# Performance work log

Hardware: AMD Instinct MI355X
Metric: run time of the kernel (lower is better)

## Reference

```python
import jax, jax.numpy as jnp
import numpy as np

B, S, D, H = 2, 2048, 2048, 16
HD = D // H


def setup_inputs() -> dict:
    key = jax.random.key(0)
    ks = jax.random.split(key, 11)
    scale = 1.0 / np.sqrt(D)
    causal = jnp.tril(jnp.ones((S, S), dtype=bool))
    attention_mask = jnp.broadcast_to(causal, (B, H, S, S))
    return {
        "queries": jax.random.normal(ks[0], (B, S, D), dtype=jnp.float32),
        "keys": jax.random.normal(ks[1], (B, S, D), dtype=jnp.float32),
        "values": jax.random.normal(ks[2], (B, S, D), dtype=jnp.float32),
        "attention_mask": attention_mask,
        "wq": jax.random.normal(ks[3], (D, D), dtype=jnp.float32) * scale,
        "bq": jax.random.normal(ks[4], (D,), dtype=jnp.float32) * 0.01,
        "wk": jax.random.normal(ks[5], (D, D), dtype=jnp.float32) * scale,
        "bk": jax.random.normal(ks[6], (D,), dtype=jnp.float32) * 0.01,
        "wv": jax.random.normal(ks[7], (D, D), dtype=jnp.float32) * scale,
        "bv": jax.random.normal(ks[8], (D,), dtype=jnp.float32) * 0.01,
        "wo": jax.random.normal(ks[9], (D, D), dtype=jnp.float32) * scale,
        "bo": jax.random.normal(ks[10], (D,), dtype=jnp.float32) * 0.01,
    }


def _split_heads(x):
    # (B, S, D) -> (B, H, S, HD)
    b, s, _ = x.shape
    return x.reshape(b, s, H, HD).transpose(0, 2, 1, 3)


def reference(queries, keys, values, attention_mask, wq, bq, wk, bk, wv, bv, wo, bo):
    # Linear layers (torch convention: x @ W.T + b)
    q = _split_heads(queries @ wq.T + bq)   # (B, H, S, HD)
    k = _split_heads(keys @ wk.T + bk)
    v = _split_heads(values @ wv.T + bv)

    inv_sqrt_d = 1.0 / jnp.sqrt(jnp.asarray(HD, dtype=q.dtype))
    scores = jnp.einsum('bhqd,bhkd->bhqk', q, k) * inv_sqrt_d  # (B, H, S, S)
    scores = jnp.where(attention_mask, scores, jnp.asarray(-jnp.inf, dtype=scores.dtype))
    probs = jax.nn.softmax(scores, axis=-1)
    out = jnp.einsum('bhqk,bhkd->bhqd', probs, v)              # (B, H, S, HD)

    out = out.transpose(0, 2, 1, 3).reshape(queries.shape[0], queries.shape[1], D)
    return out @ wo.T + bo
```

## Files before the change

### kernel.cpp

```cpp
#include <hip/hip_runtime.h>
#include <hip/hip_bf16.h>

typedef unsigned short u16;
typedef __bf16 bf16x8 __attribute__((ext_vector_type(8)));
typedef short  short8 __attribute__((ext_vector_type(8)));
typedef float  f32x4  __attribute__((ext_vector_type(4)));
typedef float  f32x16 __attribute__((ext_vector_type(16)));
typedef u16    u16x4  __attribute__((ext_vector_type(4)));

#define BB 2
#define SS 2048
#define DD 2048
#define HH 16
#define HDIM 128
#define MM (BB * SS)
#define KSCALE 0.12752039505554602f

static __device__ __forceinline__ f32x4 mfma16(short8 a, short8 b, f32x4 c) {
    return __builtin_amdgcn_mfma_f32_16x16x32_bf16(
        __builtin_bit_cast(bf16x8, a), __builtin_bit_cast(bf16x8, b), c, 0, 0, 0);
}

static __device__ __forceinline__ f32x16 mfma32(short8 a, short8 b, f32x16 c) {
    return __builtin_amdgcn_mfma_f32_32x32x16_bf16(
        __builtin_bit_cast(bf16x8, a), __builtin_bit_cast(bf16x8, b), c, 0, 0, 0);
}

static __device__ __forceinline__ u16 f2bf(float f) {
    union { float f; unsigned u; } v; v.f = f;
    unsigned r = v.u + 0x7fffu + ((v.u >> 16) & 1u);
    return (u16)(r >> 16);
}

static __device__ __forceinline__ float bf2f(u16 v) {
    union { unsigned u; float f; } t; t.u = ((unsigned)v) << 16;
    return t.f;
}

static __device__ __forceinline__ uint4 pack8(float4 a, float4 b) {
    uint4 o;
    o.x = (unsigned)f2bf(a.x) | ((unsigned)f2bf(a.y) << 16);
    o.y = (unsigned)f2bf(a.z) | ((unsigned)f2bf(a.w) << 16);
    o.z = (unsigned)f2bf(b.x) | ((unsigned)f2bf(b.y) << 16);
    o.w = (unsigned)f2bf(b.z) | ((unsigned)f2bf(b.w) << 16);
    return o;
}

static __device__ __forceinline__ void gload_lds16(const u16* g, u16* l) {
    __builtin_amdgcn_global_load_lds(
        (const __attribute__((address_space(1))) unsigned int*)g,
        (__attribute__((address_space(3))) unsigned int*)l, 16, 0, 0);
}

__global__ __launch_bounds__(256) void conv_all(
    const float* __restrict__ q, const float* __restrict__ k, const float* __restrict__ v,
    const float* __restrict__ wq, const float* __restrict__ wk,
    const float* __restrict__ wv, const float* __restrict__ wo,
    u16* __restrict__ out)
{
    constexpr int n1 = MM * DD / 8;
    constexpr int nw = DD * DD / 8;
    constexpr int total = 3 * n1 + 4 * nw;
    const int stride = gridDim.x * blockDim.x;
    for (int i = blockIdx.x * blockDim.x + threadIdx.x; i < total; i += stride) {
        const float* s; int j = i; float sc = 1.f;
        if (j < n1)            { s = q; }
        else if (j < 2 * n1)   { s = k;  j -= n1; }
        else if (j < 3 * n1)   { s = v;  j -= 2 * n1; }
        else {
            j -= 3 * n1;
            if (j < nw)        { s = wq; sc = KSCALE; }
            else if (j < 2*nw) { s = wk; j -= nw; }
            else if (j < 3*nw) { s = wv; j -= 2 * nw; }
            else               { s = wo; j -= 3 * nw; }
        }
        const float4* sp = (const float4*)s + (size_t)j * 2;
        float4 a = sp[0], bb2 = sp[1];
        a.x *= sc; a.y *= sc; a.z *= sc; a.w *= sc;
        bb2.x *= sc; bb2.y *= sc; bb2.z *= sc; bb2.w *= sc;
        ((uint4*)out)[i] = pack8(a, bb2);
    }
}

__global__ __launch_bounds__(256, 3) void gemm_qkv(
    const u16* __restrict__ A0, const u16* __restrict__ W0,
    const float* __restrict__ bq, const float* __restrict__ bk,
    const float* __restrict__ bv, u16* __restrict__ C0)
{
    __shared__ u16 S[128 * 132];
    u16* Al = S;
    u16* Bl = S + 4096;

    const int z = blockIdx.z;
    const u16* A  = A0 + (size_t)z * MM * DD;
    const u16* Wb = W0 + (size_t)z * DD * DD;
    const float* bias = (z == 0) ? bq : (z == 1 ? bk : bv);
    const float bsc = (z == 0) ? KSCALE : 1.f;

    const int tid = threadIdx.x;
    const int lane = tid & 63;
    const int lg = lane >> 4, li = lane & 15;
    const int wid = tid >> 6;
    const int brow = blockIdx.x * 128, bcol = blockIdx.y * 128;
    const int wm = wid >> 1, wn = wid & 1;

    const int srow = tid >> 2;
    const int scol = (tid & 3) * 8;

    const f32x4 zero = {0.f, 0.f, 0.f, 0.f};
    f32x4 acc[4][4];
#pragma unroll
    for (int i = 0; i < 4; ++i)
#pragma unroll
        for (int j = 0; j < 4; ++j) acc[i][j] = zero;

    const u16* aptr = A  + (size_t)(brow + srow) * DD + scol;
    const u16* bptr = Wb + (size_t)(bcol + srow) * DD + scol;
    const size_t half = (size_t)64 * DD;

    for (int kt = 0; kt < DD; kt += 32) {
        gload_lds16(aptr + kt,        &Al[tid * 8]);
        gload_lds16(aptr + half + kt, &Al[2048 + tid * 8]);
        gload_lds16(bptr + kt,        &Bl[tid * 8]);
        gload_lds16(bptr + half + kt, &Bl[2048 + tid * 8]);
        __syncthreads();

        short8 af[4], bf[4];
#pragma unroll
        for (int mi = 0; mi < 4; ++mi)
            af[mi] = *(const short8*)(&Al[(wm * 64 + mi * 16 + li) * 32 + lg * 8]);
#pragma unroll
        for (int ni = 0; ni < 4; ++ni)
            bf[ni] = *(const short8*)(&Bl[(wn * 64 + ni * 16 + li) * 32 + lg * 8]);
#pragma unroll
        for (int mi = 0; mi < 4; ++mi)
#pragma unroll
            for (int ni = 0; ni < 4; ++ni)
                acc[mi][ni] = mfma16(af[mi], bf[ni], acc[mi][ni]);
        __syncthreads();
    }

    if (z == 2) {
        u16* Cl = S;
#pragma unroll
        for (int ni = 0; ni < 4; ++ni) {
            const int cc = wn * 64 + ni * 16 + li;
            const float bvv = bias[bcol + cc];
#pragma unroll
            for (int mi = 0; mi < 4; ++mi)
#pragma unroll
                for (int r = 0; r < 4; ++r) {
                    const int rr = wm * 64 + mi * 16 + lg * 4 + r;
                    Cl[cc * 132 + rr] = f2bf(acc[mi][ni][r] + bvv);
                }
        }
        __syncthreads();
        const int row = tid >> 1;
        const int hcol = (tid & 1) * 64;
        u16* dst = C0 + (size_t)2 * MM * DD + (size_t)(bcol + row) * MM + brow + hcol;
#pragma unroll
        for (int c = 0; c < 8; ++c)
            *(short8*)(dst + c * 8) = *(const short8*)(&Cl[row * 132 + hcol + c * 8]);
    } else {
        u16* Cp = C0 + (size_t)z * MM * DD;
#pragma unroll
        for (int ni = 0; ni < 4; ++ni) {
            const int col = bcol + wn * 64 + ni * 16 + li;
            const float bvv = bias[col] * bsc;
#pragma unroll
            for (int mi = 0; mi < 4; ++mi)
#pragma unroll
                for (int r = 0; r < 4; ++r) {
                    const int row = brow + wm * 64 + mi * 16 + lg * 4 + r;
                    Cp[(size_t)row * DD + col] = f2bf(acc[mi][ni][r] + bvv);
                }
        }
    }
}

__global__ __launch_bounds__(256) void gemm_out(
    const u16* __restrict__ A, const u16* __restrict__ Wb,
    const float* __restrict__ bias, float* __restrict__ Cp)
{
    __shared__ u16 Al[128 * 32];
    __shared__ u16 Bl[128 * 32];

    const int tid = threadIdx.x;
    const int lane = tid & 63;
    const int lg = lane >> 4, li = lane & 15;
    const int wid = tid >> 6;
    const int brow = blockIdx.x * 128, bcol = blockIdx.y * 128;
    const int wm = wid >> 1, wn = wid & 1;

    const int srow = tid >> 2;
    const int scol = (tid & 3) * 8;

    const f32x4 zero = {0.f, 0.f, 0.f, 0.f};
    f32x4 acc[4][4];
#pragma unroll
    for (int i = 0; i < 4; ++i)
#pragma unroll
        for (int j = 0; j < 4; ++j) acc[i][j] = zero;

    const u16* aptr = A  + (size_t)(brow + srow) * DD + scol;
    const u16* bptr = Wb + (size_t)(bcol + srow) * DD + scol;
    const size_t half = (size_t)64 * DD;

    for (int kt = 0; kt < DD; kt += 32) {
        gload_lds16(aptr + kt,        &Al[tid * 8]);
        gload_lds16(aptr + half + kt, &Al[2048 + tid * 8]);
        gload_lds16(bptr + kt,        &Bl[tid * 8]);
        gload_lds16(bptr + half + kt, &Bl[2048 + tid * 8]);
        __syncthreads();

        short8 af[4], bf[4];
#pragma unroll
        for (int mi = 0; mi < 4; ++mi)
            af[mi] = *(const short8*)(&Al[(wm * 64 + mi * 16 + li) * 32 + lg * 8]);
#pragma unroll
        for (int ni = 0; ni < 4; ++ni)
            bf[ni] = *(const short8*)(&Bl[(wn * 64 + ni * 16 + li) * 32 + lg * 8]);
#pragma unroll
        for (int mi = 0; mi < 4; ++mi)
#pragma unroll
            for (int ni = 0; ni < 4; ++ni)
                acc[mi][ni] = mfma16(af[mi], bf[ni], acc[mi][ni]);
        __syncthreads();
    }

#pragma unroll
    for (int ni = 0; ni < 4; ++ni) {
        const int col = bcol + wn * 64 + ni * 16 + li;
        const float bvv = bias[col];
#pragma unroll
        for (int mi = 0; mi < 4; ++mi)
#pragma unroll
            for (int r = 0; r < 4; ++r) {
                const int row = brow + wm * 64 + mi * 16 + lg * 4 + r;
                Cp[(size_t)row * DD + col] = acc[mi][ni][r] + bvv;
            }
    }
}

__global__ __launch_bounds__(256) void flash_attn(
    const u16* __restrict__ Q, const u16* __restrict__ Kp,
    const u16* __restrict__ Vt, u16* __restrict__ O,
    u16* __restrict__ PartO, float* __restrict__ PartML)
{
    constexpr int SP = 72;
    __shared__ u16 lds[16384 + 4 * 32 * SP];
    u16* Kl = lds;
    u16* Vl = lds + 8192;
    u16* Pl = lds + 16384;

    const int tid = threadIdx.x;
    const int wid = tid >> 6, lane = tid & 63;
    const int l5 = lane & 31;
    const int hi = lane >> 5;
    const int h = blockIdx.y, b = blockIdx.z;

    const int f = 39 - (int)blockIdx.x;
    int qt, ch;
    if (f < 4)       { qt = f;               ch = 0; }
    else if (f < 12) { int g = f - 4;  qt = 4  + (g >> 1); ch = g & 1; }
    else if (f < 24) { int g = f - 12; qt = 8  + g / 3;    ch = g % 3; }
    else             { int g = f - 24; qt = 12 + (g >> 2); ch = g & 3; }
    const int j0 = ch * 8;
    const int j1 = min(j0 + 8, 2 * qt + 2);
    const int qbase = qt * 128 + wid * 32;
    const int qg = qbase + l5;

    const int rK0 = tid >> 4, wK0 = tid & 15;
    const int bK0 = ((wK0 * 16) ^ ((rK0 & 7) << 4)) >> 1;
    const int rV0 = tid >> 3, wV0 = tid & 7;
    const int bV0 = ((wV0 * 16) ^ ((rV0 & 7) << 4)) >> 1;
    const u16* kbase = Kp + (size_t)(b * SS + rK0) * DD + h * HDIM + bK0;
    const u16* vbase = Vt + (size_t)(h * HDIM + rV0) * MM + b * SS + bV0;

    short8 qf[8];
    {
        const u16* qp0 = Q + (size_t)(b * SS + qg) * DD + h * HDIM + hi * 8;
#pragma unroll
        for (int ks = 0; ks < 8; ++ks)
            qf[ks] = *(const short8*)(qp0 + ks * 16);
    }

    float m_r = -__builtin_inff(), l_r = 0.f;
    f32x16 accO[4];
#pragma unroll
    for (int d = 0; d < 4; ++d) accO[d] = (f32x16)(0.f);

    for (int j = j0; j < j1; ++j) {
#pragma unroll
        for (int i_ = 0; i_ < 4; ++i_) {
            gload_lds16(kbase + (size_t)(j * 64 + i_ * 16) * DD, &Kl[(i_ * 256 + tid) * 8]);
            gload_lds16(vbase + (size_t)(i_ * 32) * MM + j * 64, &Vl[(i_ * 256 + tid) * 8]);
        }
        __syncthreads();

        if (j * 64 <= qbase + 31) {
            f32x16 accS[2];
            accS[0] = (f32x16)(0.f); accS[1] = (f32x16)(0.f);
            __builtin_amdgcn_s_setprio(1);
#pragma unroll
            for (int ks = 0; ks < 8; ++ks) {
#pragma unroll
                for (int kvb = 0; kvb < 2; ++kvb) {
                    const int row = kvb * 32 + l5;
                    const int e = (ks * 16 + hi * 8) ^ ((row & 7) << 3);
                    short8 kf = *(const short8*)(&Kl[row * 128 + e]);
                    accS[kvb] = mfma32(kf, qf[ks], accS[kvb]);
                }
            }
            __builtin_amdgcn_s_setprio(0);

            const bool domask = (j * 64 + 63 > qbase);
            float rmax = -__builtin_inff();
#pragma unroll
            for (int kvb = 0; kvb < 2; ++kvb)
#pragma unroll
                for (int r = 0; r < 16; ++r) {
                    float t = accS[kvb][r];
                    const int kv = j * 64 + kvb * 32 + (r & 3) + 8 * (r >> 2) + 4 * hi;
                    if (domask && kv > qg) t = -__builtin_inff();
                    accS[kvb][r] = t;
                    rmax = fmaxf(rmax, t);
                }
            rmax = fmaxf(rmax, __shfl_xor(rmax, 32, 64));

            if (!__all(rmax - m_r <= 11.5f)) {
                const float mn = fmaxf(m_r, rmax);
                const float sf = exp2f(m_r - mn);
                m_r = mn;
                l_r *= sf;
#pragma unroll
                for (int db = 0; db < 4; ++db) accO[db] = accO[db] * sf;
            }

            float ls = 0.f;
#pragma unroll
            for (int kvb = 0; kvb < 2; ++kvb)
#pragma unroll
                for (int r = 0; r < 16; ++r) {
                    const float e = exp2f(accS[kvb][r] - m_r);
                    accS[kvb][r] = e;
                    ls += e;
                }
            ls += __shfl_xor(ls, 32, 64);
            l_r += ls;

#pragma unroll
            for (int kvb = 0; kvb < 2; ++kvb)
#pragma unroll
                for (int g = 0; g < 4; ++g) {
                    u16x4 pk;
                    pk.x = f2bf(accS[kvb][g * 4 + 0]);
                    pk.y = f2bf(accS[kvb][g * 4 + 1]);
                    pk.z = f2bf(accS[kvb][g * 4 + 2]);
                    pk.w = f2bf(accS[kvb][g * 4 + 3]);
                    *(u16x4*)(&Pl[(wid * 32 + l5) * SP + kvb * 32 + g * 8 + hi * 4]) = pk;
                }

            __builtin_amdgcn_s_setprio(1);
#pragma unroll
            for (int ks = 0; ks < 4; ++ks) {
                short8 pf = *(const short8*)(&Pl[(wid * 32 + l5) * SP + ks * 16 + hi * 8]);
#pragma unroll
                for (int db = 0; db < 4; ++db) {
                    const int row = db * 32 + l5;
                    const int e = (ks * 16 + hi * 8) ^ ((row & 7) << 3);
                    short8 vf = *(const short8*)(&Vl[row * 64 + e]);
                    accO[db] = mfma32(vf, pf, accO[db]);
                }
            }
            __builtin_amdgcn_s_setprio(0);
        }
        __syncthreads();
    }

    if (f >= 4) {
        const int pslot = (b * HH + h) * 36 + (f - 4);
        u16* po = PartO + (size_t)pslot * 16384 + (size_t)(wid * 32 + l5) * 128;
#pragma unroll
        for (int db = 0; db < 4; ++db)
#pragma unroll
            for (int g = 0; g < 4; ++g) {
                const int d0 = db * 32 + g * 8 + hi * 4;
                u16x4 pk;
                pk.x = f2bf(accO[db][g * 4 + 0]);
                pk.y = f2bf(accO[db][g * 4 + 1]);
                pk.z = f2bf(accO[db][g * 4 + 2]);
                pk.w = f2bf(accO[db][g * 4 + 3]);
                *(u16x4*)(po + d0) = pk;
            }
        if (lane < 32) {
            float* ml = PartML + (size_t)pslot * 256;
            ml[wid * 32 + l5]       = m_r;
            ml[128 + wid * 32 + l5] = l_r;
        }
    } else {
        const float linv = 1.f / l_r;
        u16* Wl = lds + wid * 4096;
#pragma unroll
        for (int db = 0; db < 4; ++db)
#pragma unroll
            for (int g = 0; g < 4; ++g) {
                const int d0 = db * 32 + g * 8 + hi * 4;
                u16x4 pk;
                pk.x = f2bf(accO[db][g * 4 + 0] * linv);
                pk.y = f2bf(accO[db][g * 4 + 1] * linv);
                pk.z = f2bf(accO[db][g * 4 + 2] * linv);
                pk.w = f2bf(accO[db][g * 4 + 3] * linv);
                *(u16x4*)(&Wl[l5 * 128 + (d0 ^ ((l5 & 7) << 4))]) = pk;
            }
        const int q_l = lane >> 1;
        const int d0r = (lane & 1) * 64;
        u16* op = O + (size_t)(b * SS + qt * 128 + wid * 32 + q_l) * DD + h * HDIM + d0r;
#pragma unroll
        for (int c = 0; c < 8; ++c) {
            short8 vv = *(const short8*)(&Wl[q_l * 128 + ((d0r + c * 8) ^ ((q_l & 7) << 4))]);
            *(short8*)(op + c * 8) = vv;
        }
    }
}

__global__ __launch_bounds__(256) void attn_combine(
    const u16* __restrict__ PartO, const float* __restrict__ PartML,
    u16* __restrict__ O)
{
    const int qt = 4 + (int)blockIdx.x;
    const int h = blockIdx.y, b = blockIdx.z;
    const int nch = qt / 4 + 1;
    int f0m4;
    if (qt < 8)       f0m4 = (qt - 4) * 2;
    else if (qt < 12) f0m4 = 8 + (qt - 8) * 3;
    else              f0m4 = 20 + (qt - 12) * 4;
    const int pbase = (b * HH + h) * 36 + f0m4;

    const int tid = threadIdx.x;
    const int q = tid & 127;
    const int d0 = (tid >> 7) * 64;

    float mc[4], lc[4];
#pragma unroll
    for (int c = 0; c < 4; ++c) {
        if (c < nch) {
            mc[c] = PartML[(size_t)(pbase + c) * 256 + q];
            lc[c] = PartML[(size_t)(pbase + c) * 256 + 128 + q];
        } else { mc[c] = -__builtin_inff(); lc[c] = 0.f; }
    }
    float M = fmaxf(fmaxf(mc[0], mc[1]), fmaxf(mc[2], mc[3]));
    float wc[4], L = 0.f;
#pragma unroll
    for (int c = 0; c < 4; ++c) { wc[c] = exp2f(mc[c] - M); L += wc[c] * lc[c]; }
    const float Linv = 1.f / L;

    float acc[64];
#pragma unroll
    for (int i = 0; i < 64; ++i) acc[i] = 0.f;
#pragma unroll
    for (int c = 0; c < 4; ++c) {
        if (c < nch) {
            const float w = wc[c] * Linv;
            const u16* po = PartO + (size_t)(pbase + c) * 16384 + (size_t)q * 128 + d0;
#pragma unroll
            for (int i = 0; i < 64; ++i)
                acc[i] += w * bf2f(po[i]);
        }
    }

    u16* op = O + (size_t)(b * SS + qt * 128 + q) * DD + h * HDIM + d0;
#pragma unroll
    for (int j = 0; j < 8; ++j) {
        short8 vv;
#pragma unroll
        for (int e = 0; e < 8; ++e) vv[e] = (short)f2bf(acc[j * 8 + e]);
        *(short8*)(op + j * 8) = vv;
    }
}

extern "C" void kernel_launch(void* const* d_in, const int* in_sizes, int n_in,
                              void* d_out, int out_size, void* d_ws, size_t ws_size,
                              hipStream_t stream)
{
    const float* queries = (const float*)d_in[0];
    const float* keys    = (const float*)d_in[1];
    const float* values  = (const float*)d_in[2];
    const float* wq = (const float*)d_in[4];
    const float* bq = (const float*)d_in[5];
    const float* wk = (const float*)d_in[6];
    const float* bk = (const float*)d_in[7];
    const float* wv = (const float*)d_in[8];
    const float* bv = (const float*)d_in[9];
    const float* wo = (const float*)d_in[10];
    const float* bo = (const float*)d_in[11];

    const int NMD = MM * DD;
    const int NWW = DD * DD;

    u16* qb  = (u16*)d_ws;
    u16* wqb = qb  + (size_t)3 * NMD;
    u16* wob = wqb + (size_t)3 * NWW;
    u16* qw  = wob + (size_t)NWW;
    u16* aw  = qw  + (size_t)3 * NMD;
    u16*   partO  = qb;
    float* partML = (float*)wqb;
    (void)in_sizes; (void)n_in; (void)out_size; (void)ws_size;

    dim3 blk(256);
    dim3 gridC(2048);
    dim3 gridQKV(MM / 128, DD / 128, 3);
    dim3 gridO(MM / 128, DD / 128);
    dim3 gridA(40, HH, BB);
    dim3 gridX(12, HH, BB);

    conv_all<<<gridC, blk, 0, stream>>>(queries, keys, values, wq, wk, wv, wo, qb);
    gemm_qkv<<<gridQKV, blk, 0, stream>>>(qb, wqb, bq, bk, bv, qw);
    flash_attn<<<gridA, blk, 0, stream>>>(qw, qw + (size_t)NMD, qw + (size_t)2 * NMD, aw,
                                          partO, partML);
    attn_combine<<<gridX, blk, 0, stream>>>(partO, partML, aw);
    gemm_out<<<gridO, blk, 0, stream>>>(aw, wob, bo, (float*)d_out);
}
```

Measured before the change: 350.8 us.

## Keep P in registers via permlane32 swap and use hardware bf16 pack conversion

```diff
diff --git a/kernel.cpp b/kernel.cpp
--- a/kernel.cpp
+++ b/kernel.cpp
@@ -7,6 +7,7 @@
 typedef float  f32x4  __attribute__((ext_vector_type(4)));
 typedef float  f32x16 __attribute__((ext_vector_type(16)));
 typedef u16    u16x4  __attribute__((ext_vector_type(4)));
+typedef unsigned uintx2 __attribute__((ext_vector_type(2)));
 
 #define BB 2
 #define SS 2048
@@ -35,6 +36,16 @@
 static __device__ __forceinline__ float bf2f(u16 v) {
     union { unsigned u; float f; } t; t.u = ((unsigned)v) << 16;
     return t.f;
+}
+
+static __device__ __forceinline__ unsigned cvtpk(float lo, float hi) {
+    unsigned r;
+    asm("v_cvt_pk_bf16_f32 %0, %1, %2" : "=v"(r) : "v"(lo), "v"(hi));
+    return r;
+}
+
+static __device__ __forceinline__ void plswap(unsigned &a, unsigned &b) {
+    asm("v_permlane32_swap_b32 %0, %1" : "+v"(a), "+v"(b));
 }
 
 static __device__ __forceinline__ uint4 pack8(float4 a, float4 b) {
@@ -247,11 +258,9 @@
     const u16* __restrict__ Vt, u16* __restrict__ O,
     u16* __restrict__ PartO, float* __restrict__ PartML)
 {
-    constexpr int SP = 72;
-    __shared__ u16 lds[16384 + 4 * 32 * SP];
+    __shared__ u16 lds[16384];
     u16* Kl = lds;
     u16* Vl = lds + 8192;
-    u16* Pl = lds + 16384;
 
     const int tid = threadIdx.x;
     const int wid = tid >> 6, lane = tid & 63;
@@ -316,16 +325,24 @@
 
             const bool domask = (j * 64 + 63 > qbase);
             float rmax = -__builtin_inff();
-#pragma unroll
-            for (int kvb = 0; kvb < 2; ++kvb)
-#pragma unroll
-                for (int r = 0; r < 16; ++r) {
-                    float t = accS[kvb][r];
-                    const int kv = j * 64 + kvb * 32 + (r & 3) + 8 * (r >> 2) + 4 * hi;
-                    if (domask && kv > qg) t = -__builtin_inff();
-                    accS[kvb][r] = t;
-                    rmax = fmaxf(rmax, t);
-                }
+            if (domask) {
+#pragma unroll
+                for (int kvb = 0; kvb < 2; ++kvb)
+#pragma unroll
+                    for (int r = 0; r < 16; ++r) {
+                        float t = accS[kvb][r];
+                        const int kv = j * 64 + kvb * 32 + (r & 3) + 8 * (r >> 2) + 4 * hi;
+                        if (kv > qg) t = -__builtin_inff();
+                        accS[kvb][r] = t;
+                        rmax = fmaxf(rmax, t);
+                    }
+            } else {
+#pragma unroll
+                for (int kvb = 0; kvb < 2; ++kvb)
+#pragma unroll
+                    for (int r = 0; r < 16; ++r)
+                        rmax = fmaxf(rmax, accS[kvb][r]);
+            }
             rmax = fmaxf(rmax, __shfl_xor(rmax, 32, 64));
 
             if (!__all(rmax - m_r <= 11.5f)) {
@@ -349,28 +366,25 @@
             ls += __shfl_xor(ls, 32, 64);
             l_r += ls;
 
-#pragma unroll
-            for (int kvb = 0; kvb < 2; ++kvb)
-#pragma unroll
-                for (int g = 0; g < 4; ++g) {
-                    u16x4 pk;
-                    pk.x = f2bf(accS[kvb][g * 4 + 0]);
-                    pk.y = f2bf(accS[kvb][g * 4 + 1]);
-                    pk.z = f2bf(accS[kvb][g * 4 + 2]);
-                    pk.w = f2bf(accS[kvb][g * 4 + 3]);
-                    *(u16x4*)(&Pl[(wid * 32 + l5) * SP + kvb * 32 + g * 8 + hi * 4]) = pk;
-                }
-
             __builtin_amdgcn_s_setprio(1);
 #pragma unroll
             for (int ks = 0; ks < 4; ++ks) {
-                short8 pf = *(const short8*)(&Pl[(wid * 32 + l5) * SP + ks * 16 + hi * 8]);
+                const int kvb = ks >> 1;
+                const int r0 = (ks & 1) * 8;
+                unsigned x0 = cvtpk(accS[kvb][r0 + 0], accS[kvb][r0 + 1]);
+                unsigned y0 = cvtpk(accS[kvb][r0 + 2], accS[kvb][r0 + 3]);
+                unsigned x1 = cvtpk(accS[kvb][r0 + 4], accS[kvb][r0 + 5]);
+                unsigned y1 = cvtpk(accS[kvb][r0 + 6], accS[kvb][r0 + 7]);
+                plswap(x0, x1);
+                plswap(y0, y1);
+                union { unsigned u[4]; short8 s; } pf;
+                pf.u[0] = x0; pf.u[1] = y0; pf.u[2] = x1; pf.u[3] = y1;
 #pragma unroll
                 for (int db = 0; db < 4; ++db) {
                     const int row = db * 32 + l5;
                     const int e = (ks * 16 + hi * 8) ^ ((row & 7) << 3);
                     short8 vf = *(const short8*)(&Vl[row * 64 + e]);
-                    accO[db] = mfma32(vf, pf, accO[db]);
+                    accO[db] = mfma32(vf, pf.s, accO[db]);
                 }
             }
             __builtin_amdgcn_s_setprio(0);
@@ -386,12 +400,10 @@
 #pragma unroll
             for (int g = 0; g < 4; ++g) {
                 const int d0 = db * 32 + g * 8 + hi * 4;
-                u16x4 pk;
-                pk.x = f2bf(accO[db][g * 4 + 0]);
-                pk.y = f2bf(accO[db][g * 4 + 1]);
-                pk.z = f2bf(accO[db][g * 4 + 2]);
-                pk.w = f2bf(accO[db][g * 4 + 3]);
-                *(u16x4*)(po + d0) = pk;
+                uintx2 pk;
+                pk.x = cvtpk(accO[db][g * 4 + 0], accO[db][g * 4 + 1]);
+                pk.y = cvtpk(accO[db][g * 4 + 2], accO[db][g * 4 + 3]);
+                *(uintx2*)(po + d0) = pk;
             }
         if (lane < 32) {
             float* ml = PartML + (size_t)pslot * 256;
@@ -406,12 +418,10 @@
 #pragma unroll
             for (int g = 0; g < 4; ++g) {
                 const int d0 = db * 32 + g * 8 + hi * 4;
-                u16x4 pk;
-                pk.x = f2bf(accO[db][g * 4 + 0] * linv);
-                pk.y = f2bf(accO[db][g * 4 + 1] * linv);
-                pk.z = f2bf(accO[db][g * 4 + 2] * linv);
-                pk.w = f2bf(accO[db][g * 4 + 3] * linv);
-                *(u16x4*)(&Wl[l5 * 128 + (d0 ^ ((l5 & 7) << 4))]) = pk;
+                uintx2 pk;
+                pk.x = cvtpk(accO[db][g * 4 + 0] * linv, accO[db][g * 4 + 1] * linv);
+                pk.y = cvtpk(accO[db][g * 4 + 2] * linv, accO[db][g * 4 + 3] * linv);
+                *(uintx2*)(&Wl[l5 * 128 + (d0 ^ ((l5 & 7) << 4))]) = pk;
             }
         const int q_l = lane >> 1;
         const int d0r = (lane & 1) * 64;
```

After: 329.4 us. 1.06x faster.
